# Kernel tuning notes

Hardware: AMD Instinct MI355X
Metric: run time of the kernel (lower is better)

## Reference

```python
import jax, jax.numpy as jnp
import numpy as np

N = 50000          # nodes
E = 800000         # edges (before self-loops)
F_IN = 128         # num_features
HID = 16           # hidden_dim (per head)
HEADS = 4
NG = 128           # number of graphs in batch
NC = 10            # num_classes
LAYERS = 3
NEG_SLOPE = 0.2    # PyG GATConv default
EPS = 1e-16


def setup_inputs() -> dict:
    key = jax.random.key(0)
    ks = jax.random.split(key, 4 + 4 * LAYERS + 2)
    inp = {}
    inp["x"] = jax.random.normal(ks[0], (N, F_IN), jnp.float32)
    inp["edge_index"] = jax.random.randint(ks[1], (2, E), 0, N, dtype=jnp.int32)
    inp["batch"] = jnp.sort(jax.random.randint(ks[2], (N,), 0, NG, dtype=jnp.int32))
    in_dims = [F_IN] + [HID * HEADS] * (LAYERS - 1)
    for i in range(LAYERS):
        kb = 3 + 4 * i
        s = 1.0 / np.sqrt(in_dims[i])
        inp[f"W{i}"] = jax.random.normal(ks[kb], (in_dims[i], HEADS * HID), jnp.float32) * s
        inp[f"b{i}"] = jnp.zeros((HEADS * HID,), jnp.float32)
        inp[f"as{i}"] = jax.random.normal(ks[kb + 1], (HEADS, HID), jnp.float32) * 0.1
        inp[f"ad{i}"] = jax.random.normal(ks[kb + 2], (HEADS, HID), jnp.float32) * 0.1
    inp["Wr"] = jax.random.normal(ks[3 + 4 * LAYERS], (HEADS * HID, NC), jnp.float32) * (1.0 / np.sqrt(HEADS * HID))
    inp["br"] = jnp.zeros((NC,), jnp.float32)
    return inp


def _gat_layer(x, src, dst, W, b, att_src, att_dst):
    n = x.shape[0]
    h = (x @ W).reshape(n, HEADS, HID)                # [N,H,D]
    a_src = jnp.einsum('nhd,hd->nh', h, att_src)      # [N,H]
    a_dst = jnp.einsum('nhd,hd->nh', h, att_dst)
    logits = jax.nn.leaky_relu(a_src[src] + a_dst[dst], NEG_SLOPE)  # [E,H]
    # segment softmax over destination node
    m = jax.ops.segment_max(logits, dst, num_segments=n)
    e = jnp.exp(logits - m[dst])
    s = jax.ops.segment_sum(e, dst, num_segments=n)
    alpha = e / (s[dst] + EPS)                        # [E,H]
    msg = h[src] * alpha[:, :, None]                  # [E,H,D]
    out = jax.ops.segment_sum(msg, dst, num_segments=n)
    return out.reshape(n, HEADS * HID) + b


def reference(x, edge_index, batch,
              W0, b0, as0, ad0,
              W1, b1, as1, ad1,
              W2, b2, as2, ad2,
              Wr, br):
    # add self loops (PyG GATConv default add_self_loops=True)
    loop = jnp.arange(N, dtype=edge_index.dtype)
    src = jnp.concatenate([edge_index[0], loop])
    dst = jnp.concatenate([edge_index[1], loop])
    params = [(W0, b0, as0, ad0), (W1, b1, as1, ad1), (W2, b2, as2, ad2)]
    h = x
    for (W, b, a_s, a_d) in params:
        h = _gat_layer(h, src, dst, W, b, a_s, a_d)
        h = jax.nn.silu(h)
        # dropout p=0.0 (eval): identity
    pooled = jax.ops.segment_sum(h, batch, num_segments=NG)   # [NG, H*D]
    logits = jax.nn.relu(pooled @ Wr + br)                    # make_mlp ends with ReLU
    return jax.nn.log_softmax(logits, axis=1)
```

## Files before the change

kernel.cpp:

```cpp
#include <hip/hip_runtime.h>
#include <cstdint>
#include <cstddef>

#define HEADS 4
#define HID 16
#define HD 64
#define NCLS 10
#define NGRAPH 128
#define NEG_SLOPE 0.2f
#define SM_EPS 1e-16f
#define SLOTS 64

static inline size_t alignup(size_t x) { return (x + 255) & ~size_t(255); }

typedef short short8 __attribute__((ext_vector_type(8)));
typedef float f32x4 __attribute__((ext_vector_type(4)));
typedef unsigned short ushort8 __attribute__((ext_vector_type(8)));

__device__ __forceinline__ unsigned short f2bf(float f) {
    return (unsigned short)((__float_as_uint(f) + 0x8000u) >> 16);
}

__global__ void scatter_kernel(const int* __restrict__ srcA, const int* __restrict__ dstA,
                               int E, int npg, int* __restrict__ cursor,
                               unsigned short* __restrict__ csr_src) {
    int g = blockIdx.x & 7;
    int c = blockIdx.x >> 3;
    int nchunks = gridDim.x >> 3;
    int chunk = (E + nchunks - 1) / nchunks;
    int start = c * chunk;
    int end = min(E, start + chunk);
    int lo = g * npg, hi = lo + npg;
    for (int e = start + threadIdx.x; e < end; e += blockDim.x) {
        int d = dstA[e];
        if (d >= lo && d < hi) {
            int pos = atomicAdd(&cursor[d], 1);
            if (pos < SLOTS) csr_src[(size_t)d * SLOTS + pos] = (unsigned short)srcA[e];
        }
    }
}

template <int K, bool INF32>
__global__ __launch_bounds__(256) void gemm_attn_kernel(
        const void* __restrict__ inp, const float* __restrict__ Wp,
        const float* __restrict__ as_, const float* __restrict__ ad_,
        unsigned short* __restrict__ hb, float* __restrict__ asrc,
        float* __restrict__ adst, int N) {
    constexpr int KP = K + 8;
    __shared__ __align__(16) unsigned short xs[64 * KP];
    __shared__ __align__(16) unsigned short wt[64 * KP];
    __shared__ float avl[HD], adl[HD];
    int tid = threadIdx.x, lane = tid & 63, wave = tid >> 6;
    if (tid < HD) { avl[tid] = as_[tid]; adl[tid] = ad_[tid]; }
    int base = blockIdx.x * 64;

    if (INF32) {
        const float* in = (const float*)inp;
        for (int i = tid; i < 64 * K / 4; i += 256) {
            int flat = i * 4;
            int r = flat / K, c = flat - r * K;
            float4 v = make_float4(0.f, 0.f, 0.f, 0.f);
            if (base + r < N) v = *(const float4*)(in + (size_t)(base + r) * K + c);
            ushort4 u;
            u.x = f2bf(v.x); u.y = f2bf(v.y); u.z = f2bf(v.z); u.w = f2bf(v.w);
            *(ushort4*)&xs[r * KP + c] = u;
        }
    } else {
        const unsigned short* in = (const unsigned short*)inp;
        for (int i = tid; i < 64 * K / 8; i += 256) {
            int flat = i * 8;
            int r = flat / K, c = flat - r * K;
            ushort8 v = (ushort8)(0);
            if (base + r < N) v = *(const ushort8*)(in + (size_t)(base + r) * K + c);
            *(ushort8*)&xs[r * KP + c] = v;
        }
    }
    for (int i = tid; i < 64 * K / 4; i += 256) {
        int flat = i * 4;
        int r = flat >> 6, c = flat & 63;
        float4 v = *(const float4*)(Wp + (size_t)r * HD + c);
        wt[(c + 0) * KP + r] = f2bf(v.x);
        wt[(c + 1) * KP + r] = f2bf(v.y);
        wt[(c + 2) * KP + r] = f2bf(v.z);
        wt[(c + 3) * KP + r] = f2bf(v.w);
    }
    __syncthreads();

    int m = lane & 15, kg = lane >> 4;
    f32x4 acc[4];
#pragma unroll
    for (int ct = 0; ct < 4; ct++) acc[ct] = (f32x4){0.f, 0.f, 0.f, 0.f};

    const unsigned short* xrow = &xs[(wave * 16 + m) * KP + kg * 8];
#pragma unroll
    for (int kb = 0; kb < K / 32; kb++) {
        short8 a = *(const short8*)(xrow + kb * 32);
#pragma unroll
        for (int ct = 0; ct < 4; ct++) {
            short8 b = *(const short8*)&wt[(ct * 16 + m) * KP + kb * 32 + kg * 8];
            acc[ct] = __builtin_amdgcn_mfma_f32_16x16x32_bf16(a, b, acc[ct], 0, 0, 0);
        }
    }

#pragma unroll
    for (int ct = 0; ct < 4; ct++) {
#pragma unroll
        for (int j = 0; j < 4; j++) {
            int node = base + wave * 16 + kg * 4 + j;
            float hv = acc[ct][j];
            float s = hv * avl[ct * 16 + m];
            float d = hv * adl[ct * 16 + m];
            s += __shfl_xor(s, 1); s += __shfl_xor(s, 2);
            s += __shfl_xor(s, 4); s += __shfl_xor(s, 8);
            d += __shfl_xor(d, 1); d += __shfl_xor(d, 2);
            d += __shfl_xor(d, 4); d += __shfl_xor(d, 8);
            if (node < N) {
                hb[(size_t)node * HD + ct * 16 + m] = f2bf(hv);
                if (m == 0) {
                    asrc[node * HEADS + ct] = s;
                    adst[node * HEADS + ct] = d;
                }
            }
        }
    }
}

__global__ void gat_gather_kernel(const int* __restrict__ deg,
                                  const unsigned short* __restrict__ csr_src,
                                  int N, const unsigned short* __restrict__ hb,
                                  const float* __restrict__ asrc, const float* __restrict__ adst,
                                  const float* __restrict__ bias, unsigned short* __restrict__ outb) {
    int wid = (int)((blockIdx.x * (long long)blockDim.x + threadIdx.x) >> 6);
    if (wid >= N) return;
    int lane = threadIdx.x & 63;
    int hh = lane & 3;
    int eg = lane >> 2;
    int e2 = lane >> 5;
    int cp = lane & 31;
    int headc = cp >> 3;

    int beg = wid * SLOTS;
    int cnt = min(deg[wid], SLOTS);
    int end = beg + cnt;

    float4 as4 = *(const float4*)&asrc[wid * 4];
    float4 ad4 = *(const float4*)&adst[wid * 4];
    float l0 = as4.x + ad4.x; l0 = l0 > 0.f ? l0 : NEG_SLOPE * l0;
    float l1 = as4.y + ad4.y; l1 = l1 > 0.f ? l1 : NEG_SLOPE * l1;
    float l2 = as4.z + ad4.z; l2 = l2 > 0.f ? l2 : NEG_SLOPE * l2;
    float l3 = as4.w + ad4.w; l3 = l3 > 0.f ? l3 : NEG_SLOPE * l3;
    float lS_hh = (hh == 0) ? l0 : (hh == 1) ? l1 : (hh == 2) ? l2 : l3;
    float ad_hh = (hh == 0) ? ad4.x : (hh == 1) ? ad4.y : (hh == 2) ? ad4.z : ad4.w;

    float dsum = 0.f;

    float2 acc2 = make_float2(0.f, 0.f);
    if (e2 == 0) {
        unsigned hw = *(const unsigned*)&hb[(unsigned)(wid * HD + 2 * cp)];
        acc2.x = __uint_as_float(hw << 16);
        acc2.y = __uint_as_float(hw & 0xffff0000u);
    }

    for (int c = beg; c < end; c += 16) {
        int e_idx = c + eg;
        unsigned pk = (unsigned)wid << 16;
        float w = 0.f;
        if (e_idx < end) {
            int s = (int)csr_src[e_idx];
            float l = asrc[(unsigned)(s * HEADS + hh)] + ad_hh;
            l = (l > 0.f) ? l : NEG_SLOPE * l;
            w = __expf(l - lS_hh);
            pk = ((unsigned)s << 16) | ((__float_as_uint(w) + 0x8000u) >> 16);
        }
        dsum += w;

        unsigned pp[8], hw[8];
#pragma unroll
        for (int j = 0; j < 8; j++) pp[j] = (unsigned)__shfl((int)pk, (e2 * 8 + j) * 4 + headc);
#pragma unroll
        for (int j = 0; j < 8; j++)
            hw[j] = *(const unsigned*)&hb[(pp[j] >> 16) * HD + 2 * cp];
#pragma unroll
        for (int j = 0; j < 8; j++) {
            float wj = __uint_as_float(pp[j] << 16);
            acc2.x += wj * __uint_as_float(hw[j] << 16);
            acc2.y += wj * __uint_as_float(hw[j] & 0xffff0000u);
        }
    }

    acc2.x += __shfl_xor(acc2.x, 32);
    acc2.y += __shfl_xor(acc2.y, 32);

    dsum += __shfl_xor(dsum, 4);
    dsum += __shfl_xor(dsum, 8);
    dsum += __shfl_xor(dsum, 16);
    dsum += __shfl_xor(dsum, 32);
    float ssum = __shfl(dsum, headc) + 1.0f;

    if (e2 == 0) {
        float2 bb2 = *(const float2*)&bias[2 * cp];
        float vx = acc2.x / (ssum + SM_EPS) + bb2.x;
        float vy = acc2.y / (ssum + SM_EPS) + bb2.y;
        float ox = vx / (1.f + expf(-vx));
        float oy = vy / (1.f + expf(-vy));
        unsigned o = (unsigned)f2bf(ox) | ((unsigned)f2bf(oy) << 16);
        *(unsigned*)&outb[(size_t)wid * HD + 2 * cp] = o;
    }
}

__global__ __launch_bounds__(256) void pool_head_kernel(
        const unsigned short* __restrict__ hx, const int* __restrict__ batch, int N,
        const float* __restrict__ Wr, const float* __restrict__ br,
        float* __restrict__ out) {
    int g = blockIdx.x;
    int tid = threadIdx.x, lane = tid & 63, wv = tid >> 6;

    int a = 0, b = N;
    while (a < b) { int m = (a + b) >> 1; if (batch[m] < g) a = m + 1; else b = m; }
    int lo = a;
    b = N;
    while (a < b) { int m = (a + b) >> 1; if (batch[m] < g + 1) a = m + 1; else b = m; }
    int hi = a;

    float acc = 0.f;
    for (int n = lo + wv; n < hi; n += 4)
        acc += __uint_as_float((unsigned)hx[(size_t)n * HD + lane] << 16);

    __shared__ float sd[4][64];
    sd[wv][lane] = acc;
    __syncthreads();
    if (wv != 0) return;

    float pooled = sd[0][lane] + sd[1][lane] + sd[2][lane] + sd[3][lane];

    float l[NCLS];
    float mx = 0.f;
#pragma unroll
    for (int c = 0; c < NCLS; c++) {
        float p = pooled * Wr[lane * NCLS + c];
#pragma unroll
        for (int off = 1; off < 64; off <<= 1) p += __shfl_xor(p, off);
        p += br[c];
        p = (p > 0.f) ? p : 0.f;
        l[c] = p;
        mx = fmaxf(mx, p);
    }
    float se = 0.f;
#pragma unroll
    for (int c = 0; c < NCLS; c++) se += __expf(l[c] - mx);
    float lse = __logf(se);
    if (lane < NCLS) out[(size_t)g * NCLS + lane] = l[lane] - mx - lse;
}

extern "C" void kernel_launch(void* const* d_in, const int* in_sizes, int n_in,
                              void* d_out, int out_size, void* d_ws, size_t ws_size,
                              hipStream_t stream) {
    const float* x = (const float*)d_in[0];
    const int* ei = (const int*)d_in[1];
    const int* batch = (const int*)d_in[2];
    const float* W[3]  = {(const float*)d_in[3], (const float*)d_in[7],  (const float*)d_in[11]};
    const float* bb[3] = {(const float*)d_in[4], (const float*)d_in[8],  (const float*)d_in[12]};
    const float* as_[3] = {(const float*)d_in[5], (const float*)d_in[9], (const float*)d_in[13]};
    const float* ad_[3] = {(const float*)d_in[6], (const float*)d_in[10], (const float*)d_in[14]};
    const float* Wr = (const float*)d_in[15];
    const float* br = (const float*)d_in[16];

    const int N = in_sizes[2];
    const int E = in_sizes[1] / 2;

    char* p = (char*)d_ws;
    unsigned short* hb = (unsigned short*)p; p += alignup((size_t)N * HD * 2);
    unsigned short* hx = (unsigned short*)p; p += alignup((size_t)N * HD * 2);
    float* asrc  = (float*)p; p += alignup((size_t)N * HEADS * 4);
    float* adst  = (float*)p; p += alignup((size_t)N * HEADS * 4);
    int* cursor  = (int*)p;   p += alignup((size_t)N * 4);
    unsigned short* csr_src = (unsigned short*)p; p += alignup((size_t)N * SLOTS * 2);

    const int* srcA = ei;
    const int* dstA = ei + E;

    int ntiles = (N + 63) / 64;
    int npg = (N + 7) / 8;
    int gather_blocks = (int)(((long long)N * 64 + 255) / 256);

    hipMemsetAsync(cursor, 0, (size_t)N * 4, stream);
    scatter_kernel<<<2048, 256, 0, stream>>>(srcA, dstA, E, npg, cursor, csr_src);

    gemm_attn_kernel<128, true><<<ntiles, 256, 0, stream>>>(x, W[0], as_[0], ad_[0],
                                                            hb, asrc, adst, N);
    gat_gather_kernel<<<gather_blocks, 256, 0, stream>>>(cursor, csr_src, N, hb,
                                                         asrc, adst, bb[0], hx);
    for (int layer = 1; layer < 3; layer++) {
        gemm_attn_kernel<64, false><<<ntiles, 256, 0, stream>>>(hx, W[layer], as_[layer],
                                                                ad_[layer], hb, asrc, adst, N);
        gat_gather_kernel<<<gather_blocks, 256, 0, stream>>>(cursor, csr_src, N, hb,
                                                             asrc, adst, bb[layer], hx);
    }

    pool_head_kernel<<<NGRAPH, 256, 0, stream>>>(hx, batch, N, Wr, br, (float*)d_out);
}
```

Measured before the change: 228.6 us.

## Fuse all GAT stages into one persistent cooperative kernel with grid syncs

Replaces the eight separate launches (scatter, three gemm+gather pairs, pooling) with a single cooperative persistent kernel that uses grid-wide barriers between phases. A fallback keeps the multi-launch path if the cooperative launch fails. The GEMM also stops staging X in shared memory and reads A fragments directly from global memory. The aim is to remove launch gaps and tail effects between kernels, at the cost of grid.sync overhead, lower occupancy from the larger shared struct, and fewer resident blocks for the latency-bound gather phase.

```diff
diff --git a/kernel.cpp b/kernel.cpp
--- a/kernel.cpp
+++ b/kernel.cpp
@@ -1,4 +1,5 @@
 #include <hip/hip_runtime.h>
+#include <hip/hip_cooperative_groups.h>
 #include <cstdint>
 #include <cstddef>
 
@@ -15,15 +16,35 @@
 
 typedef short short8 __attribute__((ext_vector_type(8)));
 typedef float f32x4 __attribute__((ext_vector_type(4)));
-typedef unsigned short ushort8 __attribute__((ext_vector_type(8)));
 
 __device__ __forceinline__ unsigned short f2bf(float f) {
     return (unsigned short)((__float_as_uint(f) + 0x8000u) >> 16);
 }
 
-__global__ void scatter_kernel(const int* __restrict__ srcA, const int* __restrict__ dstA,
-                               int E, int npg, int* __restrict__ cursor,
-                               unsigned short* __restrict__ csr_src) {
+struct MegaParams {
+    const float* x;
+    const int* srcA; const int* dstA; const int* batch;
+    const float* W0; const float* b0; const float* as0; const float* ad0;
+    const float* W1; const float* b1; const float* as1; const float* ad1;
+    const float* W2; const float* b2; const float* as2; const float* ad2;
+    const float* Wr; const float* br;
+    float* out;
+    unsigned short* hb; unsigned short* hx;
+    float* asrc; float* adst;
+    int* cursor; unsigned short* csr;
+    int N, E, ntiles, npg;
+};
+
+struct SharedBufs {
+    unsigned short wt[64 * 136];
+    float avl[HD], adl[HD];
+    float sd[4][64];
+};
+
+
+__device__ void scatter_body(const int* __restrict__ srcA, const int* __restrict__ dstA,
+                             int E, int npg, int* __restrict__ cursor,
+                             unsigned short* __restrict__ csr) {
     int g = blockIdx.x & 7;
     int c = blockIdx.x >> 3;
     int nchunks = gridDim.x >> 3;
@@ -35,186 +56,170 @@
         int d = dstA[e];
         if (d >= lo && d < hi) {
             int pos = atomicAdd(&cursor[d], 1);
-            if (pos < SLOTS) csr_src[(size_t)d * SLOTS + pos] = (unsigned short)srcA[e];
+            if (pos < SLOTS) csr[(size_t)d * SLOTS + pos] = (unsigned short)srcA[e];
         }
     }
 }
 
 template <int K, bool INF32>
-__global__ __launch_bounds__(256) void gemm_attn_kernel(
-        const void* __restrict__ inp, const float* __restrict__ Wp,
-        const float* __restrict__ as_, const float* __restrict__ ad_,
-        unsigned short* __restrict__ hb, float* __restrict__ asrc,
-        float* __restrict__ adst, int N) {
+__device__ void gemm_phase(const void* inp, const float* Wp, const float* as_,
+                           const float* ad_, unsigned short* hb, float* asrc,
+                           float* adst, int N, int ntiles, SharedBufs& sh) {
     constexpr int KP = K + 8;
-    __shared__ __align__(16) unsigned short xs[64 * KP];
-    __shared__ __align__(16) unsigned short wt[64 * KP];
-    __shared__ float avl[HD], adl[HD];
     int tid = threadIdx.x, lane = tid & 63, wave = tid >> 6;
-    if (tid < HD) { avl[tid] = as_[tid]; adl[tid] = ad_[tid]; }
-    int base = blockIdx.x * 64;
-
-    if (INF32) {
-        const float* in = (const float*)inp;
-        for (int i = tid; i < 64 * K / 4; i += 256) {
-            int flat = i * 4;
-            int r = flat / K, c = flat - r * K;
-            float4 v = make_float4(0.f, 0.f, 0.f, 0.f);
-            if (base + r < N) v = *(const float4*)(in + (size_t)(base + r) * K + c);
-            ushort4 u;
-            u.x = f2bf(v.x); u.y = f2bf(v.y); u.z = f2bf(v.z); u.w = f2bf(v.w);
-            *(ushort4*)&xs[r * KP + c] = u;
-        }
-    } else {
-        const unsigned short* in = (const unsigned short*)inp;
-        for (int i = tid; i < 64 * K / 8; i += 256) {
-            int flat = i * 8;
-            int r = flat / K, c = flat - r * K;
-            ushort8 v = (ushort8)(0);
-            if (base + r < N) v = *(const ushort8*)(in + (size_t)(base + r) * K + c);
-            *(ushort8*)&xs[r * KP + c] = v;
-        }
-    }
     for (int i = tid; i < 64 * K / 4; i += 256) {
         int flat = i * 4;
         int r = flat >> 6, c = flat & 63;
         float4 v = *(const float4*)(Wp + (size_t)r * HD + c);
-        wt[(c + 0) * KP + r] = f2bf(v.x);
-        wt[(c + 1) * KP + r] = f2bf(v.y);
-        wt[(c + 2) * KP + r] = f2bf(v.z);
-        wt[(c + 3) * KP + r] = f2bf(v.w);
-    }
+        sh.wt[(c + 0) * KP + r] = f2bf(v.x);
+        sh.wt[(c + 1) * KP + r] = f2bf(v.y);
+        sh.wt[(c + 2) * KP + r] = f2bf(v.z);
+        sh.wt[(c + 3) * KP + r] = f2bf(v.w);
+    }
+    if (tid < HD) { sh.avl[tid] = as_[tid]; sh.adl[tid] = ad_[tid]; }
     __syncthreads();
 
     int m = lane & 15, kg = lane >> 4;
-    f32x4 acc[4];
-#pragma unroll
-    for (int ct = 0; ct < 4; ct++) acc[ct] = (f32x4){0.f, 0.f, 0.f, 0.f};
-
-    const unsigned short* xrow = &xs[(wave * 16 + m) * KP + kg * 8];
-#pragma unroll
-    for (int kb = 0; kb < K / 32; kb++) {
-        short8 a = *(const short8*)(xrow + kb * 32);
+    for (int tile = blockIdx.x; tile < ntiles; tile += gridDim.x) {
+        int base = tile * 64;
+        int row = base + wave * 16 + m;
+        int rowc = min(row, N - 1);
+        f32x4 acc[4];
+#pragma unroll
+        for (int ct = 0; ct < 4; ct++) acc[ct] = (f32x4){0.f, 0.f, 0.f, 0.f};
+
+#pragma unroll
+        for (int kb = 0; kb < K / 32; kb++) {
+            short8 a;
+            if (INF32) {
+                const float* xr = (const float*)inp + (size_t)rowc * K + kb * 32 + kg * 8;
+                float4 v0 = *(const float4*)xr;
+                float4 v1 = *(const float4*)(xr + 4);
+                a[0] = (short)f2bf(v0.x); a[1] = (short)f2bf(v0.y);
+                a[2] = (short)f2bf(v0.z); a[3] = (short)f2bf(v0.w);
+                a[4] = (short)f2bf(v1.x); a[5] = (short)f2bf(v1.y);
+                a[6] = (short)f2bf(v1.z); a[7] = (short)f2bf(v1.w);
+            } else {
+                a = *(const short8*)((const unsigned short*)inp +
+                                     (size_t)rowc * K + kb * 32 + kg * 8);
+            }
+#pragma unroll
+            for (int ct = 0; ct < 4; ct++) {
+                short8 b = *(const short8*)&sh.wt[(ct * 16 + m) * KP + kb * 32 + kg * 8];
+                acc[ct] = __builtin_amdgcn_mfma_f32_16x16x32_bf16(a, b, acc[ct], 0, 0, 0);
+            }
+        }
+
 #pragma unroll
         for (int ct = 0; ct < 4; ct++) {
-            short8 b = *(const short8*)&wt[(ct * 16 + m) * KP + kb * 32 + kg * 8];
-            acc[ct] = __builtin_amdgcn_mfma_f32_16x16x32_bf16(a, b, acc[ct], 0, 0, 0);
-        }
-    }
-
-#pragma unroll
-    for (int ct = 0; ct < 4; ct++) {
-#pragma unroll
-        for (int j = 0; j < 4; j++) {
-            int node = base + wave * 16 + kg * 4 + j;
-            float hv = acc[ct][j];
-            float s = hv * avl[ct * 16 + m];
-            float d = hv * adl[ct * 16 + m];
-            s += __shfl_xor(s, 1); s += __shfl_xor(s, 2);
-            s += __shfl_xor(s, 4); s += __shfl_xor(s, 8);
-            d += __shfl_xor(d, 1); d += __shfl_xor(d, 2);
-            d += __shfl_xor(d, 4); d += __shfl_xor(d, 8);
-            if (node < N) {
-                hb[(size_t)node * HD + ct * 16 + m] = f2bf(hv);
-                if (m == 0) {
-                    asrc[node * HEADS + ct] = s;
-                    adst[node * HEADS + ct] = d;
+#pragma unroll
+            for (int j = 0; j < 4; j++) {
+                int node = base + wave * 16 + kg * 4 + j;
+                float hv = acc[ct][j];
+                float s = hv * sh.avl[ct * 16 + m];
+                float d = hv * sh.adl[ct * 16 + m];
+                s += __shfl_xor(s, 1); s += __shfl_xor(s, 2);
+                s += __shfl_xor(s, 4); s += __shfl_xor(s, 8);
+                d += __shfl_xor(d, 1); d += __shfl_xor(d, 2);
+                d += __shfl_xor(d, 4); d += __shfl_xor(d, 8);
+                if (node < N) {
+                    hb[(size_t)node * HD + ct * 16 + m] = f2bf(hv);
+                    if (m == 0) {
+                        asrc[node * HEADS + ct] = s;
+                        adst[node * HEADS + ct] = d;
+                    }
                 }
             }
         }
     }
 }
 
-__global__ void gat_gather_kernel(const int* __restrict__ deg,
-                                  const unsigned short* __restrict__ csr_src,
-                                  int N, const unsigned short* __restrict__ hb,
-                                  const float* __restrict__ asrc, const float* __restrict__ adst,
-                                  const float* __restrict__ bias, unsigned short* __restrict__ outb) {
-    int wid = (int)((blockIdx.x * (long long)blockDim.x + threadIdx.x) >> 6);
-    if (wid >= N) return;
-    int lane = threadIdx.x & 63;
-    int hh = lane & 3;
-    int eg = lane >> 2;
-    int e2 = lane >> 5;
-    int cp = lane & 31;
+__device__ void gather_phase(const int* deg, const unsigned short* csr, int N,
+                             const unsigned short* hb, const float* asrc,
+                             const float* adst, const float* bias,
+                             unsigned short* outb) {
+    int lane = threadIdx.x & 63, wave = threadIdx.x >> 6;
+    int hh = lane & 3, eg = lane >> 2, e2 = lane >> 5, cp = lane & 31;
     int headc = cp >> 3;
 
-    int beg = wid * SLOTS;
-    int cnt = min(deg[wid], SLOTS);
-    int end = beg + cnt;
-
-    float4 as4 = *(const float4*)&asrc[wid * 4];
-    float4 ad4 = *(const float4*)&adst[wid * 4];
-    float l0 = as4.x + ad4.x; l0 = l0 > 0.f ? l0 : NEG_SLOPE * l0;
-    float l1 = as4.y + ad4.y; l1 = l1 > 0.f ? l1 : NEG_SLOPE * l1;
-    float l2 = as4.z + ad4.z; l2 = l2 > 0.f ? l2 : NEG_SLOPE * l2;
-    float l3 = as4.w + ad4.w; l3 = l3 > 0.f ? l3 : NEG_SLOPE * l3;
-    float lS_hh = (hh == 0) ? l0 : (hh == 1) ? l1 : (hh == 2) ? l2 : l3;
-    float ad_hh = (hh == 0) ? ad4.x : (hh == 1) ? ad4.y : (hh == 2) ? ad4.z : ad4.w;
-
-    float dsum = 0.f;
-
-    float2 acc2 = make_float2(0.f, 0.f);
-    if (e2 == 0) {
-        unsigned hw = *(const unsigned*)&hb[(unsigned)(wid * HD + 2 * cp)];
-        acc2.x = __uint_as_float(hw << 16);
-        acc2.y = __uint_as_float(hw & 0xffff0000u);
-    }
-
-    for (int c = beg; c < end; c += 16) {
-        int e_idx = c + eg;
-        unsigned pk = (unsigned)wid << 16;
-        float w = 0.f;
-        if (e_idx < end) {
-            int s = (int)csr_src[e_idx];
-            float l = asrc[(unsigned)(s * HEADS + hh)] + ad_hh;
-            l = (l > 0.f) ? l : NEG_SLOPE * l;
-            w = __expf(l - lS_hh);
-            pk = ((unsigned)s << 16) | ((__float_as_uint(w) + 0x8000u) >> 16);
-        }
-        dsum += w;
-
-        unsigned pp[8], hw[8];
-#pragma unroll
-        for (int j = 0; j < 8; j++) pp[j] = (unsigned)__shfl((int)pk, (e2 * 8 + j) * 4 + headc);
-#pragma unroll
-        for (int j = 0; j < 8; j++)
-            hw[j] = *(const unsigned*)&hb[(pp[j] >> 16) * HD + 2 * cp];
-#pragma unroll
-        for (int j = 0; j < 8; j++) {
-            float wj = __uint_as_float(pp[j] << 16);
-            acc2.x += wj * __uint_as_float(hw[j] << 16);
-            acc2.y += wj * __uint_as_float(hw[j] & 0xffff0000u);
-        }
-    }
-
-    acc2.x += __shfl_xor(acc2.x, 32);
-    acc2.y += __shfl_xor(acc2.y, 32);
-
-    dsum += __shfl_xor(dsum, 4);
-    dsum += __shfl_xor(dsum, 8);
-    dsum += __shfl_xor(dsum, 16);
-    dsum += __shfl_xor(dsum, 32);
-    float ssum = __shfl(dsum, headc) + 1.0f;
-
-    if (e2 == 0) {
-        float2 bb2 = *(const float2*)&bias[2 * cp];
-        float vx = acc2.x / (ssum + SM_EPS) + bb2.x;
-        float vy = acc2.y / (ssum + SM_EPS) + bb2.y;
-        float ox = vx / (1.f + expf(-vx));
-        float oy = vy / (1.f + expf(-vy));
-        unsigned o = (unsigned)f2bf(ox) | ((unsigned)f2bf(oy) << 16);
-        *(unsigned*)&outb[(size_t)wid * HD + 2 * cp] = o;
-    }
-}
-
-__global__ __launch_bounds__(256) void pool_head_kernel(
-        const unsigned short* __restrict__ hx, const int* __restrict__ batch, int N,
-        const float* __restrict__ Wr, const float* __restrict__ br,
-        float* __restrict__ out) {
-    int g = blockIdx.x;
+    for (int nb = blockIdx.x; nb * 4 < N; nb += gridDim.x) {
+        int wid = nb * 4 + wave;
+        if (wid >= N) continue;
+
+        int beg = wid * SLOTS;
+        int cnt = min(deg[wid], SLOTS);
+        int end = beg + cnt;
+
+        float4 as4 = *(const float4*)&asrc[wid * 4];
+        float4 ad4 = *(const float4*)&adst[wid * 4];
+        float l0 = as4.x + ad4.x; l0 = l0 > 0.f ? l0 : NEG_SLOPE * l0;
+        float l1 = as4.y + ad4.y; l1 = l1 > 0.f ? l1 : NEG_SLOPE * l1;
+        float l2 = as4.z + ad4.z; l2 = l2 > 0.f ? l2 : NEG_SLOPE * l2;
+        float l3 = as4.w + ad4.w; l3 = l3 > 0.f ? l3 : NEG_SLOPE * l3;
+        float lS_hh = (hh == 0) ? l0 : (hh == 1) ? l1 : (hh == 2) ? l2 : l3;
+        float ad_hh = (hh == 0) ? ad4.x : (hh == 1) ? ad4.y : (hh == 2) ? ad4.z : ad4.w;
+
+        float dsum = 0.f;
+        float2 acc2 = make_float2(0.f, 0.f);
+        if (e2 == 0) {
+            unsigned hw = *(const unsigned*)&hb[(unsigned)(wid * HD + 2 * cp)];
+            acc2.x = __uint_as_float(hw << 16);
+            acc2.y = __uint_as_float(hw & 0xffff0000u);
+        }
+
+        for (int c = beg; c < end; c += 16) {
+            int e_idx = c + eg;
+            unsigned pk = (unsigned)wid << 16;
+            float w = 0.f;
+            if (e_idx < end) {
+                int s = (int)csr[e_idx];
+                float l = asrc[(unsigned)(s * HEADS + hh)] + ad_hh;
+                l = (l > 0.f) ? l : NEG_SLOPE * l;
+                w = __expf(l - lS_hh);
+                pk = ((unsigned)s << 16) | ((__float_as_uint(w) + 0x8000u) >> 16);
+            }
+            dsum += w;
+
+            unsigned pp[8], hw[8];
+#pragma unroll
+            for (int j = 0; j < 8; j++)
+                pp[j] = (unsigned)__shfl((int)pk, (e2 * 8 + j) * 4 + headc);
+#pragma unroll
+            for (int j = 0; j < 8; j++)
+                hw[j] = *(const unsigned*)&hb[(pp[j] >> 16) * HD + 2 * cp];
+#pragma unroll
+            for (int j = 0; j < 8; j++) {
+                float wj = __uint_as_float(pp[j] << 16);
+                acc2.x += wj * __uint_as_float(hw[j] << 16);
+                acc2.y += wj * __uint_as_float(hw[j] & 0xffff0000u);
+            }
+        }
+
+        acc2.x += __shfl_xor(acc2.x, 32);
+        acc2.y += __shfl_xor(acc2.y, 32);
+
+        dsum += __shfl_xor(dsum, 4);
+        dsum += __shfl_xor(dsum, 8);
+        dsum += __shfl_xor(dsum, 16);
+        dsum += __shfl_xor(dsum, 32);
+        float ssum = __shfl(dsum, headc) + 1.0f;
+
+        if (e2 == 0) {
+            float2 bb2 = *(const float2*)&bias[2 * cp];
+            float vx = acc2.x / (ssum + SM_EPS) + bb2.x;
+            float vy = acc2.y / (ssum + SM_EPS) + bb2.y;
+            float ox = vx / (1.f + expf(-vx));
+            float oy = vy / (1.f + expf(-vy));
+            unsigned o = (unsigned)f2bf(ox) | ((unsigned)f2bf(oy) << 16);
+            *(unsigned*)&outb[(size_t)wid * HD + 2 * cp] = o;
+        }
+    }
+}
+
+__device__ void pool_head_body(const unsigned short* hx, const int* batch, int N,
+                               const float* Wr, const float* br, float* out,
+                               int g, float (*sd)[64]) {
     int tid = threadIdx.x, lane = tid & 63, wv = tid >> 6;
-
     int a = 0, b = N;
     while (a < b) { int m = (a + b) >> 1; if (batch[m] < g) a = m + 1; else b = m; }
     int lo = a;
@@ -226,24 +231,22 @@
     for (int n = lo + wv; n < hi; n += 4)
         acc += __uint_as_float((unsigned)hx[(size_t)n * HD + lane] << 16);
 
-    __shared__ float sd[4][64];
     sd[wv][lane] = acc;
     __syncthreads();
     if (wv != 0) return;
 
     float pooled = sd[0][lane] + sd[1][lane] + sd[2][lane] + sd[3][lane];
-
     float l[NCLS];
     float mx = 0.f;
 #pragma unroll
     for (int c = 0; c < NCLS; c++) {
-        float p = pooled * Wr[lane * NCLS + c];
-#pragma unroll
-        for (int off = 1; off < 64; off <<= 1) p += __shfl_xor(p, off);
-        p += br[c];
-        p = (p > 0.f) ? p : 0.f;
-        l[c] = p;
-        mx = fmaxf(mx, p);
+        float pp = pooled * Wr[lane * NCLS + c];
+#pragma unroll
+        for (int off = 1; off < 64; off <<= 1) pp += __shfl_xor(pp, off);
+        pp += br[c];
+        pp = (pp > 0.f) ? pp : 0.f;
+        l[c] = pp;
+        mx = fmaxf(mx, pp);
     }
     float se = 0.f;
 #pragma unroll
@@ -252,19 +255,58 @@
     if (lane < NCLS) out[(size_t)g * NCLS + lane] = l[lane] - mx - lse;
 }
 
+__global__ __launch_bounds__(256) void mega_kernel(MegaParams p) {
+    cooperative_groups::grid_group grid = cooperative_groups::this_grid();
+    __shared__ SharedBufs sh;
+
+    scatter_body(p.srcA, p.dstA, p.E, p.npg, p.cursor, p.csr);
+    grid.sync();
+
+    gemm_phase<128, true>(p.x, p.W0, p.as0, p.ad0, p.hb, p.asrc, p.adst, p.N, p.ntiles, sh);
+    grid.sync();
+    gather_phase(p.cursor, p.csr, p.N, p.hb, p.asrc, p.adst, p.b0, p.hx);
+    grid.sync();
+    __syncthreads();
+    gemm_phase<64, false>(p.hx, p.W1, p.as1, p.ad1, p.hb, p.asrc, p.adst, p.N, p.ntiles, sh);
+    grid.sync();
+    gather_phase(p.cursor, p.csr, p.N, p.hb, p.asrc, p.adst, p.b1, p.hx);
+    grid.sync();
+    __syncthreads();
+    gemm_phase<64, false>(p.hx, p.W2, p.as2, p.ad2, p.hb, p.asrc, p.adst, p.N, p.ntiles, sh);
+    grid.sync();
+    gather_phase(p.cursor, p.csr, p.N, p.hb, p.asrc, p.adst, p.b2, p.hx);
+    grid.sync();
+
+    if (blockIdx.x < NGRAPH)
+        pool_head_body(p.hx, p.batch, p.N, p.Wr, p.br, p.out, blockIdx.x, sh.sd);
+}
+
+__global__ __launch_bounds__(256) void scatter_kernel(MegaParams p) {
+    scatter_body(p.srcA, p.dstA, p.E, p.npg, p.cursor, p.csr);
+}
+template <int K, bool INF32>
+__global__ __launch_bounds__(256) void gemm_attn_kernel(
+        const void* inp, const float* Wp, const float* as_, const float* ad_,
+        unsigned short* hb, float* asrc, float* adst, int N, int ntiles) {
+    __shared__ SharedBufs sh;
+    gemm_phase<K, INF32>(inp, Wp, as_, ad_, hb, asrc, adst, N, ntiles, sh);
+}
+__global__ void gat_gather_kernel(const int* deg, const unsigned short* csr, int N,
+                                  const unsigned short* hb, const float* asrc,
+                                  const float* adst, const float* bias,
+                                  unsigned short* outb) {
+    gather_phase(deg, csr, N, hb, asrc, adst, bias, outb);
+}
+__global__ __launch_bounds__(256) void pool_head_kernel(
+        const unsigned short* hx, const int* batch, int N,
+        const float* Wr, const float* br, float* out) {
+    __shared__ float sd[4][64];
+    pool_head_body(hx, batch, N, Wr, br, out, blockIdx.x, sd);
+}
+
 extern "C" void kernel_launch(void* const* d_in, const int* in_sizes, int n_in,
                               void* d_out, int out_size, void* d_ws, size_t ws_size,
                               hipStream_t stream) {
-    const float* x = (const float*)d_in[0];
-    const int* ei = (const int*)d_in[1];
-    const int* batch = (const int*)d_in[2];
-    const float* W[3]  = {(const float*)d_in[3], (const float*)d_in[7],  (const float*)d_in[11]};
-    const float* bb[3] = {(const float*)d_in[4], (const float*)d_in[8],  (const float*)d_in[12]};
-    const float* as_[3] = {(const float*)d_in[5], (const float*)d_in[9], (const float*)d_in[13]};
-    const float* ad_[3] = {(const float*)d_in[6], (const float*)d_in[10], (const float*)d_in[14]};
-    const float* Wr = (const float*)d_in[15];
-    const float* br = (const float*)d_in[16];
-
     const int N = in_sizes[2];
     const int E = in_sizes[1] / 2;
 
@@ -276,26 +318,57 @@
     int* cursor  = (int*)p;   p += alignup((size_t)N * 4);
     unsigned short* csr_src = (unsigned short*)p; p += alignup((size_t)N * SLOTS * 2);
 
-    const int* srcA = ei;
-    const int* dstA = ei + E;
-
-    int ntiles = (N + 63) / 64;
-    int npg = (N + 7) / 8;
-    int gather_blocks = (int)(((long long)N * 64 + 255) / 256);
+    MegaParams mp;
+    mp.x = (const float*)d_in[0];
+    mp.srcA = (const int*)d_in[1];
+    mp.dstA = (const int*)d_in[1] + E;
+    mp.batch = (const int*)d_in[2];
+    mp.W0 = (const float*)d_in[3];  mp.b0 = (const float*)d_in[4];
+    mp.as0 = (const float*)d_in[5]; mp.ad0 = (const float*)d_in[6];
+    mp.W1 = (const float*)d_in[7];  mp.b1 = (const float*)d_in[8];
+    mp.as1 = (const float*)d_in[9]; mp.ad1 = (const float*)d_in[10];
+    mp.W2 = (const float*)d_in[11]; mp.b2 = (const float*)d_in[12];
+    mp.as2 = (const float*)d_in[13]; mp.ad2 = (const float*)d_in[14];
+    mp.Wr = (const float*)d_in[15]; mp.br = (const float*)d_in[16];
+    mp.out = (float*)d_out;
+    mp.hb = hb; mp.hx = hx;
+    mp.asrc = asrc; mp.adst = adst;
+    mp.cursor = cursor; mp.csr = csr_src;
+    mp.N = N; mp.E = E;
+    mp.ntiles = (N + 63) / 64;
+    mp.npg = (N + 7) / 8;
 
     hipMemsetAsync(cursor, 0, (size_t)N * 4, stream);
-    scatter_kernel<<<2048, 256, 0, stream>>>(srcA, dstA, E, npg, cursor, csr_src);
-
-    gemm_attn_kernel<128, true><<<ntiles, 256, 0, stream>>>(x, W[0], as_[0], ad_[0],
-                                                            hb, asrc, adst, N);
-    gat_gather_kernel<<<gather_blocks, 256, 0, stream>>>(cursor, csr_src, N, hb,
-                                                         asrc, adst, bb[0], hx);
-    for (int layer = 1; layer < 3; layer++) {
-        gemm_attn_kernel<64, false><<<ntiles, 256, 0, stream>>>(hx, W[layer], as_[layer],
-                                                                ad_[layer], hb, asrc, adst, N);
+
+    int dev = 0, nCU = 0, perCU = 0;
+    hipGetDevice(&dev);
+    hipDeviceGetAttribute(&nCU, hipDeviceAttributeMultiprocessorCount, dev);
+    hipOccupancyMaxActiveBlocksPerMultiprocessor(&perCU, (const void*)mega_kernel, 256, 0);
+    int grid = (perCU * nCU) & ~7;
+
+    hipError_t rc = hipErrorUnknown;
+    if (grid >= NGRAPH) {
+        void* kp[] = { &mp };
+        rc = hipLaunchCooperativeKernel((const void*)mega_kernel, dim3(grid), dim3(256),
+                                        kp, 0, stream);
+    }
+    if (rc != hipSuccess) {
+        int ntiles = mp.ntiles;
+        int gather_blocks = (N + 3) / 4;
+        scatter_kernel<<<2048, 256, 0, stream>>>(mp);
+        gemm_attn_kernel<128, true><<<ntiles, 256, 0, stream>>>(
+            mp.x, mp.W0, mp.as0, mp.ad0, hb, asrc, adst, N, ntiles);
         gat_gather_kernel<<<gather_blocks, 256, 0, stream>>>(cursor, csr_src, N, hb,
-                                                             asrc, adst, bb[layer], hx);
-    }
-
-    pool_head_kernel<<<NGRAPH, 256, 0, stream>>>(hx, batch, N, Wr, br, (float*)d_out);
-}
+                                                             asrc, adst, mp.b0, hx);
+        gemm_attn_kernel<64, false><<<ntiles, 256, 0, stream>>>(
+            hx, mp.W1, mp.as1, mp.ad1, hb, asrc, adst, N, ntiles);
+        gat_gather_kernel<<<gather_blocks, 256, 0, stream>>>(cursor, csr_src, N, hb,
+                                                             asrc, adst, mp.b1, hx);
+        gemm_attn_kernel<64, false><<<ntiles, 256, 0, stream>>>(
+            hx, mp.W2, mp.as2, mp.ad2, hb, asrc, adst, N, ntiles);
+        gat_gather_kernel<<<gather_blocks, 256, 0, stream>>>(cursor, csr_src, N, hb,
+                                                             asrc, adst, mp.b2, hx);
+        pool_head_kernel<<<NGRAPH, 256, 0, stream>>>(hx, mp.batch, N, mp.Wr, mp.br,
+                                                     (float*)d_out);
+    }
+}
```

Result: slower. 762.8 us (+233.7%).
